# Kernel optimization log

Measured on AMD Instinct MI355X. Metric: run time of the kernel, lower is better.

The kernel has to match this reference:

```python
import jax, jax.numpy as jnp
import numpy as np

N, M, D = 20000, 16000, 128

def setup_inputs() -> dict:
    key = jax.random.key(0)
    ks = jax.random.split(key, 4)
    return {
        "clear_feature": jax.random.normal(ks[0], (N, D), dtype=jnp.float32),
        "rain_feature": jax.random.normal(ks[1], (M, D), dtype=jnp.float32),
        # torch nn.Linear weight layout: (out_features, in_features)
        "W1": jax.random.normal(ks[2], (D, 2 * D), dtype=jnp.float32) * 0.05,
        "b1": jnp.zeros((D,), dtype=jnp.float32),
        "W2": jax.random.normal(ks[3], (1, D), dtype=jnp.float32) * 0.05,
        "b2": jnp.zeros((1,), dtype=jnp.float32),
    }

def reference(clear_feature, rain_feature, W1, b1, W2, b2):
    # --- KNN alignment (k=1): argmin of squared Euclidean distance == cdist+topk(smallest) ---
    x2 = jnp.sum(clear_feature * clear_feature, axis=-1, keepdims=True)   # [N,1]
    y2 = jnp.sum(rain_feature * rain_feature, axis=-1)                    # [M]
    d2 = x2 + y2 - 2.0 * (clear_feature @ rain_feature.T)                 # [N,M]
    idx = jnp.argmin(d2, axis=-1)                                         # [N]
    aligned = rain_feature[idx]                                           # [N,D] gather
    # --- attention MLP: Linear(2D->D) + ReLU + Linear(D->1) + Sigmoid ---
    comb = jnp.concatenate([clear_feature, aligned], axis=-1)             # [N,2D]
    h = jax.nn.relu(comb @ W1.T + b1)                                     # [N,D]
    w = jax.nn.sigmoid(h @ W2.T + b2)                                     # [N,1]
    # --- gated fusion ---
    return w * clear_feature + (1.0 - w) * aligned
```

## Files before the change

kernel.cpp:

```cpp
#include <hip/hip_runtime.h>
#include <stdint.h>

#define NN 20000
#define MM 16000
#define DD 128
#define CT2 250
#define SPLITS 32
#define RB 79

typedef unsigned long long u64;
typedef _Float16 f16x8 __attribute__((ext_vector_type(8)));
typedef float f32x16 __attribute__((ext_vector_type(16)));

__global__ void k_y2(const float* __restrict__ rain, float* __restrict__ y2) {
    int row = blockIdx.x * 4 + (threadIdx.x >> 6);
    int lane = threadIdx.x & 63;
    if (row >= MM) return;
    float2 v = ((const float2*)(rain + (size_t)row * DD))[lane];
    float s = v.x * v.x + v.y * v.y;
    #pragma unroll
    for (int off = 32; off > 0; off >>= 1) s += __shfl_down(s, off);
    if (lane == 0) y2[row] = s;
}

__global__ void k_split_B(const float* __restrict__ rain, _Float16* __restrict__ Bimg) {
    int id = blockIdx.x * 256 + threadIdx.x;
    if (id >= CT2 * 1024) return;
    int cl = id & 31;
    int cg = (id >> 5) & 1;
    int kp = (id >> 6) & 15;
    int tc = id >> 10;
    int row = tc * 64 + cg * 32 + cl;
    const float4* src = (const float4*)(rain + (size_t)row * DD + kp * 8);
    float4 v0 = src[0], v1 = src[1];
    float x[8] = {v0.x, v0.y, v0.z, v0.w, v1.x, v1.y, v1.z, v1.w};
    _Float16 hi[8], lo[8];
    #pragma unroll
    for (int j = 0; j < 8; ++j) {
        _Float16 h = (_Float16)x[j];
        hi[j] = h;
        lo[j] = (_Float16)(x[j] - (float)h);
    }
    int ks = kp >> 1, kh = kp & 1;
    int chunk = ((ks * 2 + cg) * 2 + kh) * 32 + cl;
    size_t base = (size_t)tc * 16384;
    *(f16x8*)(Bimg + base + (size_t)chunk * 8) = *(f16x8*)hi;
    *(f16x8*)(Bimg + base + 8192 + (size_t)chunk * 8) = *(f16x8*)lo;
}

__global__ void k_w1img(const float* __restrict__ W1, _Float16* __restrict__ W1img) {
    int id = blockIdx.x * 256 + threadIdx.x;
    if (id >= 4096) return;
    int cl = id & 31;
    int kh = (id >> 5) & 1;
    int cg = (id >> 6) & 3;
    int ks = id >> 8;
    int d = cg * 32 + cl;
    int k = ks * 16 + kh * 8;
    const float4* src = (const float4*)(W1 + (size_t)d * 256 + k);
    float4 v0 = src[0], v1 = src[1];
    float x[8] = {v0.x, v0.y, v0.z, v0.w, v1.x, v1.y, v1.z, v1.w};
    _Float16 h[8];
    #pragma unroll
    for (int j = 0; j < 8; ++j) h[j] = (_Float16)x[j];
    *(f16x8*)(W1img + (size_t)id * 8) = *(f16x8*)h;
}

__global__ __launch_bounds__(256, 2) void k_dist(
        const float* __restrict__ clear_f,
        const _Float16* __restrict__ Bimg, const float* __restrict__ y2,
        u64* __restrict__ keys2) {
    __shared__ _Float16 lds[2][16384];
    __shared__ float y2s[512];

    const int tid = threadIdx.x;
    const int w = tid >> 6, lane = tid & 63;
    const int l5 = lane >> 5, l31 = lane & 31;
    const int b = blockIdx.x;
    const int split = b & 31;
    const int n0 = (b >> 5) * 256;
    const int nt = (CT2 - split + SPLITS - 1) / SPLITS;

    {
        const _Float16* gsrc = Bimg + (size_t)split * 16384;
        #pragma unroll
        for (int n = 0; n < 8; ++n) {
            int seg = w * 8 + n;
            __builtin_amdgcn_global_load_lds(
                (const __attribute__((address_space(1))) unsigned int*)
                    (gsrc + (size_t)seg * 512 + (size_t)lane * 8),
                (__attribute__((address_space(3))) unsigned int*)
                    (&lds[0][0] + (size_t)seg * 512),
                16, 0, 0);
        }
    }

    for (int j = tid; j < nt * 64; j += 256) {
        int tt = j >> 6;
        int cc = j & 63;
        y2s[j] = y2[(split + tt * SPLITS) * 64 + cc];
    }

    f16x8 afh[2][8], afl[2][8];
    #pragma unroll
    for (int rb = 0; rb < 2; ++rb) {
        int r = n0 + w * 64 + rb * 32 + l31;
        if (r >= NN) r = NN - 1;
        const float* ap = clear_f + (size_t)r * DD + l5 * 8;
        #pragma unroll
        for (int ks = 0; ks < 8; ++ks) {
            float4 v0 = *(const float4*)(ap + ks * 16);
            float4 v1 = *(const float4*)(ap + ks * 16 + 4);
            float x[8] = {v0.x, v0.y, v0.z, v0.w, v1.x, v1.y, v1.z, v1.w};
            _Float16 hi[8], lo[8];
            #pragma unroll
            for (int j = 0; j < 8; ++j) {
                float s = -2.f * x[j];
                _Float16 h = (_Float16)s;
                hi[j] = h;
                lo[j] = (_Float16)(s - (float)h);
            }
            afh[rb][ks] = *(f16x8*)hi;
            afl[rb][ks] = *(f16x8*)lo;
        }
    }

    __syncthreads();

    float bestd[32];
    unsigned bits[4] = {0u, 0u, 0u, 0u};
    #pragma unroll
    for (int s = 0; s < 32; ++s) bestd[s] = 1e30f;

    int p = 0;
    for (int i = 0; i < nt; ++i) {
        const int t = split + i * SPLITS;

        if (i + 1 < nt) {
            const _Float16* gsrc = Bimg + (size_t)(t + SPLITS) * 16384;
            _Float16* dst = &lds[1 - p][0];
            #pragma unroll
            for (int n = 0; n < 8; ++n) {
                int seg = w * 8 + n;
                __builtin_amdgcn_global_load_lds(
                    (const __attribute__((address_space(1))) unsigned int*)
                        (gsrc + (size_t)seg * 512 + (size_t)lane * 8),
                    (__attribute__((address_space(3))) unsigned int*)
                        (dst + (size_t)seg * 512),
                    16, 0, 0);
            }
        }

        float y2v0 = y2s[i * 64 + l31];
        float y2v1 = y2s[i * 64 + 32 + l31];

        f32x16 acc00, acc01, acc10, acc11;
        #pragma unroll
        for (int e = 0; e < 16; ++e) {
            acc00[e] = y2v0; acc10[e] = y2v0;
            acc01[e] = y2v1; acc11[e] = y2v1;
        }

        const _Float16* lbuf = &lds[p][0];
        #pragma unroll
        for (int ks = 0; ks < 8; ++ks) {
            f16x8 bh0 = *(const f16x8*)(lbuf + (size_t)(ks * 2 + 0) * 512 + (size_t)lane * 8);
            f16x8 bh1 = *(const f16x8*)(lbuf + (size_t)(ks * 2 + 1) * 512 + (size_t)lane * 8);
            f16x8 bl0 = *(const f16x8*)(lbuf + 8192 + (size_t)(ks * 2 + 0) * 512 + (size_t)lane * 8);
            f16x8 bl1 = *(const f16x8*)(lbuf + 8192 + (size_t)(ks * 2 + 1) * 512 + (size_t)lane * 8);
            acc00 = __builtin_amdgcn_mfma_f32_32x32x16_f16(afh[0][ks], bh0, acc00, 0, 0, 0);
            acc10 = __builtin_amdgcn_mfma_f32_32x32x16_f16(afh[1][ks], bh0, acc10, 0, 0, 0);
            acc01 = __builtin_amdgcn_mfma_f32_32x32x16_f16(afh[0][ks], bh1, acc01, 0, 0, 0);
            acc11 = __builtin_amdgcn_mfma_f32_32x32x16_f16(afh[1][ks], bh1, acc11, 0, 0, 0);
            acc00 = __builtin_amdgcn_mfma_f32_32x32x16_f16(afh[0][ks], bl0, acc00, 0, 0, 0);
            acc10 = __builtin_amdgcn_mfma_f32_32x32x16_f16(afh[1][ks], bl0, acc10, 0, 0, 0);
            acc01 = __builtin_amdgcn_mfma_f32_32x32x16_f16(afh[0][ks], bl1, acc01, 0, 0, 0);
            acc11 = __builtin_amdgcn_mfma_f32_32x32x16_f16(afh[1][ks], bl1, acc11, 0, 0, 0);
            acc00 = __builtin_amdgcn_mfma_f32_32x32x16_f16(afl[0][ks], bh0, acc00, 0, 0, 0);
            acc10 = __builtin_amdgcn_mfma_f32_32x32x16_f16(afl[1][ks], bh0, acc10, 0, 0, 0);
            acc01 = __builtin_amdgcn_mfma_f32_32x32x16_f16(afl[0][ks], bh1, acc01, 0, 0, 0);
            acc11 = __builtin_amdgcn_mfma_f32_32x32x16_f16(afl[1][ks], bh1, acc11, 0, 0, 0);
        }

        const unsigned ibase = (unsigned)i << 1;
        #pragma unroll
        for (int e = 0; e < 16; ++e) {
            {
                float d0 = acc00[e], d1 = acc01[e];
                bool tk = d1 < d0;
                float dm = tk ? d1 : d0;
                int s = e, sh = 4 * (e & 7);
                bool up = dm < bestd[s];
                bestd[s] = up ? dm : bestd[s];
                unsigned nib = ibase | (unsigned)tk;
                bits[s >> 3] = up ? ((bits[s >> 3] & ~(15u << sh)) | (nib << sh))
                                  : bits[s >> 3];
            }
            {
                float d0 = acc10[e], d1 = acc11[e];
                bool tk = d1 < d0;
                float dm = tk ? d1 : d0;
                int s = 16 + e, sh = 4 * (s & 7);
                bool up = dm < bestd[s];
                bestd[s] = up ? dm : bestd[s];
                unsigned nib = ibase | (unsigned)tk;
                bits[s >> 3] = up ? ((bits[s >> 3] & ~(15u << sh)) | (nib << sh))
                                  : bits[s >> 3];
            }
        }

        __syncthreads();
        p ^= 1;
    }

    #pragma unroll
    for (int s = 0; s < 32; ++s) {
        unsigned nib = (bits[s >> 3] >> (4 * (s & 7))) & 15u;
        int i4 = (int)(nib >> 1), cg = (int)(nib & 1);
        int col = (split + i4 * SPLITS) * 64 + cg * 32 + l31;
        unsigned u = __float_as_uint(bestd[s]);
        u = (u & 0x80000000u) ? ~u : (u | 0x80000000u);
        u64 key = ((u64)u << 32) | (unsigned)col;
        #pragma unroll
        for (int off = 1; off < 32; off <<= 1) {
            u64 o = __shfl_xor(key, off);
            if (o < key) key = o;
        }
        if (l31 == 0) {
            int e = s & 15, rb = s >> 4;
            int grow = n0 + w * 64 + rb * 32 + (e & 3) + 8 * (e >> 2) + 4 * l5;
            if (grow < NN) keys2[(size_t)grow * SPLITS + split] = key;
        }
    }
}

__global__ void k_reduce(const u64* __restrict__ keys2, int* __restrict__ idx) {
    int n = blockIdx.x * 256 + threadIdx.x;
    if (n >= NN) return;
    const u64* p = keys2 + (size_t)n * SPLITS;
    u64 best = ~0ull;
    #pragma unroll
    for (int j = 0; j < SPLITS; ++j) {
        u64 k = p[j];
        if (k < best) best = k;
    }
    idx[n] = (int)(best & 0xffffffffu);
}

__global__ __launch_bounds__(256, 2) void k_mlp(
        const float* __restrict__ clear_f, const float* __restrict__ rain_f,
        const _Float16* __restrict__ W1img, const float* __restrict__ b1,
        const float* __restrict__ W2, const float* __restrict__ b2,
        const int* __restrict__ idx, float* __restrict__ out) {
    __shared__ _Float16 w1s[32768];

    const int tid = threadIdx.x;
    const int w = tid >> 6, lane = tid & 63;
    const int l5 = lane >> 5, l31 = lane & 31;
    const int n0 = blockIdx.x * 128;

    #pragma unroll
    for (int n = 0; n < 16; ++n) {
        int seg = w * 16 + n;
        __builtin_amdgcn_global_load_lds(
            (const __attribute__((address_space(1))) unsigned int*)
                (W1img + (size_t)seg * 512 + (size_t)lane * 8),
            (__attribute__((address_space(3))) unsigned int*)
                (&w1s[0] + (size_t)seg * 512),
            16, 0, 0);
    }

    int n = n0 + w * 32 + l31;
    int nc = n < NN ? n : NN - 1;
    int rid = idx[nc];
    f16x8 af[16];
    #pragma unroll
    for (int ks = 0; ks < 16; ++ks) {
        int k0 = ks * 16 + l5 * 8;
        const float4* src = (k0 < 128)
            ? (const float4*)(clear_f + (size_t)nc * DD + k0)
            : (const float4*)(rain_f + (size_t)rid * DD + (k0 - 128));
        float4 v0 = src[0], v1 = src[1];
        float x[8] = {v0.x, v0.y, v0.z, v0.w, v1.x, v1.y, v1.z, v1.w};
        _Float16 h[8];
        #pragma unroll
        for (int j = 0; j < 8; ++j) h[j] = (_Float16)x[j];
        af[ks] = *(f16x8*)h;
    }

    __syncthreads();

    f32x16 acc[4];
    #pragma unroll
    for (int cg = 0; cg < 4; ++cg)
        #pragma unroll
        for (int e = 0; e < 16; ++e) acc[cg][e] = 0.f;

    #pragma unroll
    for (int ks = 0; ks < 16; ++ks) {
        #pragma unroll
        for (int cg = 0; cg < 4; ++cg) {
            f16x8 bh = *(const f16x8*)(&w1s[0] +
                ((size_t)((ks * 4 + cg) * 2 + l5)) * 256 + (size_t)l31 * 8);
            acc[cg] = __builtin_amdgcn_mfma_f32_32x32x16_f16(af[ks], bh, acc[cg], 0, 0, 0);
        }
    }

    float b1v[4], w2v[4];
    #pragma unroll
    for (int cg = 0; cg < 4; ++cg) {
        b1v[cg] = b1[cg * 32 + l31];
        w2v[cg] = W2[cg * 32 + l31];
    }
    float b2v = b2[0];

    #pragma unroll
    for (int e = 0; e < 16; ++e) {
        float part = 0.f;
        #pragma unroll
        for (int cg = 0; cg < 4; ++cg) {
            float hv = acc[cg][e] + b1v[cg];
            hv = hv > 0.f ? hv : 0.f;
            part = fmaf(hv, w2v[cg], part);
        }
        #pragma unroll
        for (int off = 1; off < 32; off <<= 1) part += __shfl_xor(part, off);
        float s = part + b2v;
        float wv = 1.f / (1.f + expf(-s));
        int row = n0 + w * 32 + (e & 3) + 8 * (e >> 2) + 4 * l5;
        if (row < NN) {
            int rid2 = idx[row];
            float4 cv = *(const float4*)(clear_f + (size_t)row * DD + l31 * 4);
            float4 av = *(const float4*)(rain_f + (size_t)rid2 * DD + l31 * 4);
            float4 ov;
            ov.x = wv * cv.x + (1.f - wv) * av.x;
            ov.y = wv * cv.y + (1.f - wv) * av.y;
            ov.z = wv * cv.z + (1.f - wv) * av.z;
            ov.w = wv * cv.w + (1.f - wv) * av.w;
            *(float4*)(out + (size_t)row * DD + l31 * 4) = ov;
        }
    }
}

extern "C" void kernel_launch(void* const* d_in, const int* in_sizes, int n_in,
                              void* d_out, int out_size, void* d_ws, size_t ws_size,
                              hipStream_t stream) {
    const float* clear_f = (const float*)d_in[0];
    const float* rain_f = (const float*)d_in[1];
    const float* W1 = (const float*)d_in[2];
    const float* b1 = (const float*)d_in[3];
    const float* W2 = (const float*)d_in[4];
    const float* b2 = (const float*)d_in[5];
    float* out = (float*)d_out;

    char* ws = (char*)d_ws;
    u64* keys2 = (u64*)ws;
    int* idx = (int*)(ws + 5120000);
    float* y2 = (float*)(ws + 5200000);
    _Float16* Bimg = (_Float16*)(ws + 5264000);
    _Float16* W1img = (_Float16*)(ws + 13456000);

    k_y2<<<MM / 4, 256, 0, stream>>>(rain_f, y2);
    k_split_B<<<(CT2 * 1024 + 255) / 256, 256, 0, stream>>>(rain_f, Bimg);
    k_w1img<<<16, 256, 0, stream>>>(W1, W1img);
    k_dist<<<RB * SPLITS, 256, 0, stream>>>(clear_f, Bimg, y2, keys2);
    k_reduce<<<(NN + 255) / 256, 256, 0, stream>>>(keys2, idx);
    k_mlp<<<(NN + 127) / 128, 256, 0, stream>>>(clear_f, rain_f, W1img, b1, W2, b2, idx, out);
}
```

Baseline: 346.6 us.

## Merge prep kernels and fold split-reduce into single-wave MLP kernel

```diff
diff --git a/kernel.cpp b/kernel.cpp
--- a/kernel.cpp
+++ b/kernel.cpp
@@ -12,58 +12,59 @@
 typedef _Float16 f16x8 __attribute__((ext_vector_type(8)));
 typedef float f32x16 __attribute__((ext_vector_type(16)));
 
-__global__ void k_y2(const float* __restrict__ rain, float* __restrict__ y2) {
-    int row = blockIdx.x * 4 + (threadIdx.x >> 6);
-    int lane = threadIdx.x & 63;
-    if (row >= MM) return;
-    float2 v = ((const float2*)(rain + (size_t)row * DD))[lane];
-    float s = v.x * v.x + v.y * v.y;
-    #pragma unroll
-    for (int off = 32; off > 0; off >>= 1) s += __shfl_down(s, off);
-    if (lane == 0) y2[row] = s;
-}
-
-__global__ void k_split_B(const float* __restrict__ rain, _Float16* __restrict__ Bimg) {
-    int id = blockIdx.x * 256 + threadIdx.x;
-    if (id >= CT2 * 1024) return;
-    int cl = id & 31;
-    int cg = (id >> 5) & 1;
-    int kp = (id >> 6) & 15;
-    int tc = id >> 10;
-    int row = tc * 64 + cg * 32 + cl;
-    const float4* src = (const float4*)(rain + (size_t)row * DD + kp * 8);
-    float4 v0 = src[0], v1 = src[1];
-    float x[8] = {v0.x, v0.y, v0.z, v0.w, v1.x, v1.y, v1.z, v1.w};
-    _Float16 hi[8], lo[8];
-    #pragma unroll
-    for (int j = 0; j < 8; ++j) {
-        _Float16 h = (_Float16)x[j];
-        hi[j] = h;
-        lo[j] = (_Float16)(x[j] - (float)h);
-    }
-    int ks = kp >> 1, kh = kp & 1;
-    int chunk = ((ks * 2 + cg) * 2 + kh) * 32 + cl;
-    size_t base = (size_t)tc * 16384;
-    *(f16x8*)(Bimg + base + (size_t)chunk * 8) = *(f16x8*)hi;
-    *(f16x8*)(Bimg + base + 8192 + (size_t)chunk * 8) = *(f16x8*)lo;
-}
-
-__global__ void k_w1img(const float* __restrict__ W1, _Float16* __restrict__ W1img) {
-    int id = blockIdx.x * 256 + threadIdx.x;
-    if (id >= 4096) return;
-    int cl = id & 31;
-    int kh = (id >> 5) & 1;
-    int cg = (id >> 6) & 3;
-    int ks = id >> 8;
-    int d = cg * 32 + cl;
-    int k = ks * 16 + kh * 8;
-    const float4* src = (const float4*)(W1 + (size_t)d * 256 + k);
-    float4 v0 = src[0], v1 = src[1];
-    float x[8] = {v0.x, v0.y, v0.z, v0.w, v1.x, v1.y, v1.z, v1.w};
-    _Float16 h[8];
-    #pragma unroll
-    for (int j = 0; j < 8; ++j) h[j] = (_Float16)x[j];
-    *(f16x8*)(W1img + (size_t)id * 8) = *(f16x8*)h;
+__global__ void k_prep(const float* __restrict__ rain, const float* __restrict__ W1,
+                       float* __restrict__ y2, _Float16* __restrict__ Bimg,
+                       _Float16* __restrict__ W1img) {
+    const int bb = blockIdx.x;
+    const int tid = threadIdx.x;
+    if (bb < 4000) {
+        int row = bb * 4 + (tid >> 6);
+        int lane = tid & 63;
+        if (row >= MM) return;
+        float2 v = ((const float2*)(rain + (size_t)row * DD))[lane];
+        float s = v.x * v.x + v.y * v.y;
+        #pragma unroll
+        for (int off = 32; off > 0; off >>= 1) s += __shfl_down(s, off);
+        if (lane == 0) y2[row] = s;
+    } else if (bb < 5000) {
+        int id = (bb - 4000) * 256 + tid;
+        int cl = id & 31;
+        int cg = (id >> 5) & 1;
+        int kp = (id >> 6) & 15;
+        int tc = id >> 10;
+        int row = tc * 64 + cg * 32 + cl;
+        const float4* src = (const float4*)(rain + (size_t)row * DD + kp * 8);
+        float4 v0 = src[0], v1 = src[1];
+        float x[8] = {v0.x, v0.y, v0.z, v0.w, v1.x, v1.y, v1.z, v1.w};
+        _Float16 hi[8], lo[8];
+        #pragma unroll
+        for (int j = 0; j < 8; ++j) {
+            _Float16 h = (_Float16)x[j];
+            hi[j] = h;
+            lo[j] = (_Float16)(x[j] - (float)h);
+        }
+        int ks = kp >> 1, kh = kp & 1;
+        int chunk = ((ks * 2 + cg) * 2 + kh) * 32 + cl;
+        size_t base = (size_t)tc * 16384;
+        *(f16x8*)(Bimg + base + (size_t)chunk * 8) = *(f16x8*)hi;
+        *(f16x8*)(Bimg + base + 8192 + (size_t)chunk * 8) = *(f16x8*)lo;
+    } else {
+        int id = (bb - 5000) * 256 + tid;
+        if (id >= 4096) return;
+        int cl = id & 31;
+        int kh = (id >> 5) & 1;
+        int cg = (id >> 6) & 3;
+        int ks = id >> 8;
+        int d = cg * 32 + cl;
+        int k = ks * 16 + kh * 8;
+        const float4* src = (const float4*)(W1 + (size_t)d * 256 + k);
+        float4 v0 = src[0], v1 = src[1];
+        float x[8] = {v0.x, v0.y, v0.z, v0.w, v1.x, v1.y, v1.z, v1.w};
+        _Float16 h[8];
+        #pragma unroll
+        for (int j = 0; j < 8; ++j) h[j] = (_Float16)x[j];
+        *(f16x8*)(W1img + (size_t)id * 8) = *(f16x8*)h;
+    }
 }
 
 __global__ __launch_bounds__(256, 2) void k_dist(
@@ -234,45 +235,34 @@
     }
 }
 
-__global__ void k_reduce(const u64* __restrict__ keys2, int* __restrict__ idx) {
-    int n = blockIdx.x * 256 + threadIdx.x;
-    if (n >= NN) return;
-    const u64* p = keys2 + (size_t)n * SPLITS;
-    u64 best = ~0ull;
-    #pragma unroll
-    for (int j = 0; j < SPLITS; ++j) {
-        u64 k = p[j];
-        if (k < best) best = k;
-    }
-    idx[n] = (int)(best & 0xffffffffu);
-}
-
-__global__ __launch_bounds__(256, 2) void k_mlp(
+__global__ __launch_bounds__(64) void k_mlp(
         const float* __restrict__ clear_f, const float* __restrict__ rain_f,
         const _Float16* __restrict__ W1img, const float* __restrict__ b1,
         const float* __restrict__ W2, const float* __restrict__ b2,
-        const int* __restrict__ idx, float* __restrict__ out) {
-    __shared__ _Float16 w1s[32768];
-
-    const int tid = threadIdx.x;
-    const int w = tid >> 6, lane = tid & 63;
+        const u64* __restrict__ keys2, float* __restrict__ out) {
+    __shared__ int idxs[32];
+
+    const int lane = threadIdx.x;
     const int l5 = lane >> 5, l31 = lane & 31;
-    const int n0 = blockIdx.x * 128;
-
-    #pragma unroll
-    for (int n = 0; n < 16; ++n) {
-        int seg = w * 16 + n;
-        __builtin_amdgcn_global_load_lds(
-            (const __attribute__((address_space(1))) unsigned int*)
-                (W1img + (size_t)seg * 512 + (size_t)lane * 8),
-            (__attribute__((address_space(3))) unsigned int*)
-                (&w1s[0] + (size_t)seg * 512),
-            16, 0, 0);
-    }
-
-    int n = n0 + w * 32 + l31;
-    int nc = n < NN ? n : NN - 1;
-    int rid = idx[nc];
+    const int n0 = blockIdx.x * 32;
+
+    {
+        int r = lane >> 1;
+        const u64* pk = keys2 + (size_t)(n0 + r) * SPLITS + (lane & 1) * 16;
+        u64 best = pk[0];
+        #pragma unroll
+        for (int t = 1; t < 16; ++t) {
+            u64 k2 = pk[t];
+            if (k2 < best) best = k2;
+        }
+        u64 o = __shfl_xor(best, 1);
+        if (o < best) best = o;
+        if ((lane & 1) == 0) idxs[r] = (int)(best & 0xffffffffu);
+    }
+    __syncthreads();
+
+    int nc = n0 + l31;
+    int rid = idxs[l31];
     f16x8 af[16];
     #pragma unroll
     for (int ks = 0; ks < 16; ++ks) {
@@ -288,8 +278,6 @@
         af[ks] = *(f16x8*)h;
     }
 
-    __syncthreads();
-
     f32x16 acc[4];
     #pragma unroll
     for (int cg = 0; cg < 4; ++cg)
@@ -300,7 +288,7 @@
     for (int ks = 0; ks < 16; ++ks) {
         #pragma unroll
         for (int cg = 0; cg < 4; ++cg) {
-            f16x8 bh = *(const f16x8*)(&w1s[0] +
+            f16x8 bh = *(const f16x8*)(W1img +
                 ((size_t)((ks * 4 + cg) * 2 + l5)) * 256 + (size_t)l31 * 8);
             acc[cg] = __builtin_amdgcn_mfma_f32_32x32x16_f16(af[ks], bh, acc[cg], 0, 0, 0);
         }
@@ -327,18 +315,16 @@
         for (int off = 1; off < 32; off <<= 1) part += __shfl_xor(part, off);
         float s = part + b2v;
         float wv = 1.f / (1.f + expf(-s));
-        int row = n0 + w * 32 + (e & 3) + 8 * (e >> 2) + 4 * l5;
-        if (row < NN) {
-            int rid2 = idx[row];
-            float4 cv = *(const float4*)(clear_f + (size_t)row * DD + l31 * 4);
-            float4 av = *(const float4*)(rain_f + (size_t)rid2 * DD + l31 * 4);
-            float4 ov;
-            ov.x = wv * cv.x + (1.f - wv) * av.x;
-            ov.y = wv * cv.y + (1.f - wv) * av.y;
-            ov.z = wv * cv.z + (1.f - wv) * av.z;
-            ov.w = wv * cv.w + (1.f - wv) * av.w;
-            *(float4*)(out + (size_t)row * DD + l31 * 4) = ov;
-        }
+        int row = n0 + (e & 3) + 8 * (e >> 2) + 4 * l5;
+        int rid2 = idxs[row - n0];
+        float4 cv = *(const float4*)(clear_f + (size_t)row * DD + l31 * 4);
+        float4 av = *(const float4*)(rain_f + (size_t)rid2 * DD + l31 * 4);
+        float4 ov;
+        ov.x = wv * cv.x + (1.f - wv) * av.x;
+        ov.y = wv * cv.y + (1.f - wv) * av.y;
+        ov.z = wv * cv.z + (1.f - wv) * av.z;
+        ov.w = wv * cv.w + (1.f - wv) * av.w;
+        *(float4*)(out + (size_t)row * DD + l31 * 4) = ov;
     }
 }
 
@@ -355,15 +341,11 @@
 
     char* ws = (char*)d_ws;
     u64* keys2 = (u64*)ws;
-    int* idx = (int*)(ws + 5120000);
-    float* y2 = (float*)(ws + 5200000);
-    _Float16* Bimg = (_Float16*)(ws + 5264000);
-    _Float16* W1img = (_Float16*)(ws + 13456000);
-
-    k_y2<<<MM / 4, 256, 0, stream>>>(rain_f, y2);
-    k_split_B<<<(CT2 * 1024 + 255) / 256, 256, 0, stream>>>(rain_f, Bimg);
-    k_w1img<<<16, 256, 0, stream>>>(W1, W1img);
+    float* y2 = (float*)(ws + 5120000);
+    _Float16* Bimg = (_Float16*)(ws + 5184000);
+    _Float16* W1img = (_Float16*)(ws + 13376000);
+
+    k_prep<<<5016, 256, 0, stream>>>(rain_f, W1, y2, Bimg, W1img);
     k_dist<<<RB * SPLITS, 256, 0, stream>>>(clear_f, Bimg, y2, keys2);
-    k_reduce<<<(NN + 255) / 256, 256, 0, stream>>>(keys2, idx);
-    k_mlp<<<(NN + 127) / 128, 256, 0, stream>>>(clear_f, rain_f, W1img, b1, W2, b2, idx, out);
+    k_mlp<<<NN / 32, 64, 0, stream>>>(clear_f, rain_f, W1img, b1, W2, b2, keys2, out);
 }
```

New measurement: 342.1 us (median of 2 runs). Within noise of the previous version (-1.3%).
